# Optimization experiments

Hardware: AMD Instinct MI355X
Metric: run time of the kernel (lower is better)

## Reference

```python
import jax, jax.numpy as jnp
import numpy as np

N_QUBITS = 10


def _apply_1q(state, U, wire, n):
    # state: (B, 2**n) complex; apply 2x2 U on `wire` (wire 0 = most significant bit)
    B = state.shape[0]
    left = 2 ** wire
    right = 2 ** (n - wire - 1)
    s = state.reshape(B, left, 2, right)
    s = jnp.einsum('ij,bljr->blir', U, s)
    return s.reshape(B, 2 ** n)


def _cnot(state, c, t, n):
    # CNOT with control wire c, target wire t
    B = state.shape[0]
    s = state.reshape((B,) + (2,) * n)
    ci, ti = c + 1, t + 1
    flipped = jnp.flip(s, axis=ti)
    zero = jnp.take(s, 0, axis=ci)      # control=0 slice unchanged
    one = jnp.take(flipped, 1, axis=ci)  # control=1 slice with target flipped
    s = jnp.stack([zero, one], axis=ci)
    return s.reshape(B, 2 ** n)


def _rot_matrix(phi, theta, omega):
    # PennyLane Rot(phi, theta, omega) = RZ(omega) @ RY(theta) @ RZ(phi)
    c = jnp.cos(theta / 2).astype(jnp.complex64)
    s = jnp.sin(theta / 2).astype(jnp.complex64)
    ep = jnp.exp(-0.5j * (phi + omega).astype(jnp.complex64))  # e^{-i(phi+omega)/2}
    em = jnp.exp(0.5j * (phi - omega).astype(jnp.complex64))   # e^{ i(phi-omega)/2}
    row0 = jnp.stack([ep * c, -em * s])
    row1 = jnp.stack([jnp.conj(em) * s, jnp.conj(ep) * c])
    return jnp.stack([row0, row1])  # (2, 2)


def setup_inputs() -> dict:
    key = jax.random.key(0)
    k1, k2 = jax.random.split(key)
    B, dim = 8192, 2 ** N_QUBITS
    patch = jax.random.normal(k1, (B, dim), dtype=jnp.float32)
    patch = patch / jnp.linalg.norm(patch, axis=1, keepdims=True)  # L2-normalized amplitudes
    weights = 0.01 * jax.random.normal(k2, (N_QUBITS, 3), dtype=jnp.float32)
    return {"patch_batch": patch, "weights": weights}


def reference(patch_batch, weights):
    n = weights.shape[0]
    state = patch_batch.astype(jnp.complex64)  # amplitude embedding
    for w in range(n):
        U = _rot_matrix(weights[w, 0], weights[w, 1], weights[w, 2])
        state = _apply_1q(state, U, w, n)
    for w in range(n - 1):
        state = _cnot(state, w, w + 1, n)
    state = _cnot(state, n - 1, 0, n)
    # expectation values of X, Y, Z on wire 0
    s2 = state.reshape(-1, 2, 2 ** (n - 1))
    a0, a1 = s2[:, 0], s2[:, 1]
    z = jnp.sum(jnp.conj(a0) * a1, axis=1)
    ex = 2.0 * jnp.real(z)
    ey = 2.0 * jnp.imag(z)
    ez = jnp.sum(jnp.abs(a0) ** 2 - jnp.abs(a1) ** 2, axis=1)
    out = jnp.stack([ex, ey, ez], axis=1)  # (B, 3)
    return jnp.nan_to_num(out, nan=0.0, posinf=1.0, neginf=-1.0)
```

## Files before the change

### kernel.cpp

```cpp
#include <hip/hip_runtime.h>


__global__ void qk_setup_gates(const float* __restrict__ w, float* __restrict__ U) {
    int i = threadIdx.x;
    if (i < 10) {
        float phi = w[3 * i + 0];
        float th  = w[3 * i + 1];
        float om  = w[3 * i + 2];
        float c  = cosf(0.5f * th), s  = sinf(0.5f * th);
        float hp = 0.5f * (phi + om), hm = 0.5f * (phi - om);
        float chp = cosf(hp), shp = sinf(hp);
        float chm = cosf(hm), shm = sinf(hm);
        float* u = U + 8 * i;
        u[0] =  c * chp;  u[1] = -c * shp;
        u[2] = -s * chm;  u[3] = -s * shm;
        u[4] =  s * chm;  u[5] = -s * shm;
        u[6] =  c * chp;  u[7] =  c * shp;
    }
}

__global__ __launch_bounds__(256) void qk_sim(const float* __restrict__ x,
                                              const float* __restrict__ Ug,
                                              float* __restrict__ out,
                                              int nstates) {
    int wave = (int)((blockIdx.x * blockDim.x + threadIdx.x) >> 6);
    int lane = threadIdx.x & 63;
    if (wave >= nstates) return;

    const float4* row = (const float4*)(x + (size_t)wave * 1024);
    float re[16], im[16];
#pragma unroll
    for (int k = 0; k < 4; k++) {
        float4 v = row[lane * 4 + k];
        re[4 * k + 0] = v.x; re[4 * k + 1] = v.y;
        re[4 * k + 2] = v.z; re[4 * k + 3] = v.w;
        im[4 * k + 0] = 0.f; im[4 * k + 1] = 0.f;
        im[4 * k + 2] = 0.f; im[4 * k + 3] = 0.f;
    }

#pragma unroll
    for (int rb = 0; rb < 4; rb++) {
        const float* u = Ug + 8 * (9 - rb);
        float u0 = u[0], u1 = u[1], u2 = u[2], u3 = u[3];
        float u4 = u[4], u5 = u[5], u6 = u[6], u7 = u[7];
#pragma unroll
        for (int r0 = 0; r0 < 16; r0++) {
            if (r0 & (1 << rb)) continue;
            int r1 = r0 | (1 << rb);
            float ar = re[r0], ai = im[r0];
            float br = re[r1], bi = im[r1];
            re[r0] = u0 * ar - u1 * ai + u2 * br - u3 * bi;
            im[r0] = u0 * ai + u1 * ar + u2 * bi + u3 * br;
            re[r1] = u4 * ar - u5 * ai + u6 * br - u7 * bi;
            im[r1] = u4 * ai + u5 * ar + u6 * bi + u7 * br;
        }
    }

#pragma unroll
    for (int l = 0; l < 6; l++) {
        const float* u = Ug + 8 * (5 - l);
        int bit = (lane >> l) & 1;
        float Ar = bit ? u[6] : u[0];
        float Ai = bit ? u[7] : u[1];
        float Br = bit ? u[4] : u[2];
        float Bi = bit ? u[5] : u[3];
#pragma unroll
        for (int r = 0; r < 16; r++) {
            float mr = re[r], mi = im[r];
            float pr = __shfl_xor(mr, 1 << l, 64);
            float pi = __shfl_xor(mi, 1 << l, 64);
            re[r] = Ar * mr - Ai * mi + Br * pr - Bi * pi;
            im[r] = Ar * mi + Ai * mr + Br * pi + Bi * pr;
        }
    }

    float ex = 0.f, ey = 0.f, ez = 0.f;
    int lpar = __popc(lane & 31) & 1;
#pragma unroll
    for (int r = 0; r < 16; r++) {
        float mr = re[r], mi = im[r];
        float pr = __shfl_xor(mr, 48, 64);
        float pi = __shfl_xor(mi, 48, 64);
        float sgn = ((lpar ^ (__popc(r) & 1)) != 0) ? -1.f : 1.f;
        ex += mr * pr + mi * pi;
        ey += sgn * (mr * pi - mi * pr);
        ez += sgn * (mr * mr + mi * mi);
    }
#pragma unroll
    for (int off = 32; off >= 1; off >>= 1) {
        ex += __shfl_xor(ex, off, 64);
        ey += __shfl_xor(ey, off, 64);
        ez += __shfl_xor(ez, off, 64);
    }
    if (lane == 0) {
        float* o = out + 3 * (size_t)wave;
        o[0] = ex; o[1] = ey; o[2] = ez;
    }
}

extern "C" void kernel_launch(void* const* d_in, const int* in_sizes, int n_in,
                              void* d_out, int out_size, void* d_ws, size_t ws_size,
                              hipStream_t stream) {
    const float* patch   = (const float*)d_in[0];
    const float* weights = (const float*)d_in[1];
    float* out = (float*)d_out;
    float* Ug  = (float*)d_ws;

    int nstates = in_sizes[0] / 1024;

    qk_setup_gates<<<1, 64, 0, stream>>>(weights, Ug);

    int waves_per_block = 256 / 64;
    int nblocks = (nstates + waves_per_block - 1) / waves_per_block;
    qk_sim<<<nblocks, 256, 0, stream>>>(patch, Ug, out, nstates);
}
```

Before: 94.98 us.

## Factor Rot gates into diagonal phases plus real RY rotations

Each Rot gate is split into its RZ phase parts and a real RY rotation. The RZ(phi) phases act on a real input state, so they fold into one precomputed per-lane and per-register phase multiply at load time. The RY butterflies become real 2x2 mixes, roughly quartering the FLOPs per amplitude pair, and the final RZ(omega) phases are applied only to the partial sums of the wire-0 expectations. The block count also drops its rounding-up, so the launch assumes the state count is a multiple of four.

Result: no change. 93.89 us (-1.1%).

```diff
diff --git a/kernel.cpp b/kernel.cpp
--- a/kernel.cpp
+++ b/kernel.cpp
@@ -1,100 +1,120 @@
 #include <hip/hip_runtime.h>
 
 
-__global__ void qk_setup_gates(const float* __restrict__ w, float* __restrict__ U) {
-    int i = threadIdx.x;
-    if (i < 10) {
-        float phi = w[3 * i + 0];
-        float th  = w[3 * i + 1];
-        float om  = w[3 * i + 2];
-        float c  = cosf(0.5f * th), s  = sinf(0.5f * th);
-        float hp = 0.5f * (phi + om), hm = 0.5f * (phi - om);
-        float chp = cosf(hp), shp = sinf(hp);
-        float chm = cosf(hm), shm = sinf(hm);
-        float* u = U + 8 * i;
-        u[0] =  c * chp;  u[1] = -c * shp;
-        u[2] = -s * chm;  u[3] = -s * shm;
-        u[4] =  s * chm;  u[5] = -s * shm;
-        u[6] =  c * chp;  u[7] =  c * shp;
+__global__ void qk_setup(const float* __restrict__ w, float* __restrict__ ws) {
+    int t = threadIdx.x;
+    if (t < 10) {
+        float th = w[3 * t + 1];
+        ws[2 * t]     = cosf(0.5f * th);
+        ws[2 * t + 1] = sinf(0.5f * th);
+    }
+    if (t < 16) {
+        float a = 0.f;
+        for (int j = 0; j < 4; j++) if ((t >> j) & 1) a += w[3 * (9 - j)];
+        ws[32 + 2 * t]     = cosf(a);
+        ws[32 + 2 * t + 1] = sinf(a);
+    }
+    {
+        float a = 0.f;
+        for (int j = 0; j < 6; j++) if ((t >> j) & 1) a += w[3 * (5 - j)];
+        ws[64 + 2 * t]     = cosf(a);
+        ws[64 + 2 * t + 1] = sinf(a);
+    }
+    if (t < 4) {
+        float d = (1.f - 2.f * ((t >> 1) & 1)) * w[2] + (1.f - 2.f * (t & 1)) * w[5];
+        ws[192 + 2 * t]     = cosf(d);
+        ws[192 + 2 * t + 1] = sinf(d);
     }
 }
 
 __global__ __launch_bounds__(256) void qk_sim(const float* __restrict__ x,
-                                              const float* __restrict__ Ug,
+                                              const float* __restrict__ ws,
                                               float* __restrict__ out,
                                               int nstates) {
     int wave = (int)((blockIdx.x * blockDim.x + threadIdx.x) >> 6);
     int lane = threadIdx.x & 63;
     if (wave >= nstates) return;
 
+    const float* CS = ws;
+    const float* R  = ws + 32;
+    const float* L  = ws + 64;
+    const float* T4 = ws + 192;
+
+    float Lr = L[2 * lane], Li = L[2 * lane + 1];
+
     const float4* row = (const float4*)(x + (size_t)wave * 1024);
     float re[16], im[16];
 #pragma unroll
     for (int k = 0; k < 4; k++) {
         float4 v = row[lane * 4 + k];
-        re[4 * k + 0] = v.x; re[4 * k + 1] = v.y;
-        re[4 * k + 2] = v.z; re[4 * k + 3] = v.w;
-        im[4 * k + 0] = 0.f; im[4 * k + 1] = 0.f;
-        im[4 * k + 2] = 0.f; im[4 * k + 3] = 0.f;
+        float xs0 = v.x, xs1 = v.y, xs2 = v.z, xs3 = v.w;
+        float xv[4] = {xs0, xs1, xs2, xs3};
+#pragma unroll
+        for (int j = 0; j < 4; j++) {
+            int r = 4 * k + j;
+            float ar = xv[j] * R[2 * r];
+            float ai = xv[j] * R[2 * r + 1];
+            re[r] = Lr * ar - Li * ai;
+            im[r] = Lr * ai + Li * ar;
+        }
     }
 
 #pragma unroll
     for (int rb = 0; rb < 4; rb++) {
-        const float* u = Ug + 8 * (9 - rb);
-        float u0 = u[0], u1 = u[1], u2 = u[2], u3 = u[3];
-        float u4 = u[4], u5 = u[5], u6 = u[6], u7 = u[7];
+        float c = CS[2 * (9 - rb)], s = CS[2 * (9 - rb) + 1];
 #pragma unroll
         for (int r0 = 0; r0 < 16; r0++) {
             if (r0 & (1 << rb)) continue;
             int r1 = r0 | (1 << rb);
-            float ar = re[r0], ai = im[r0];
-            float br = re[r1], bi = im[r1];
-            re[r0] = u0 * ar - u1 * ai + u2 * br - u3 * bi;
-            im[r0] = u0 * ai + u1 * ar + u2 * bi + u3 * br;
-            re[r1] = u4 * ar - u5 * ai + u6 * br - u7 * bi;
-            im[r1] = u4 * ai + u5 * ar + u6 * bi + u7 * br;
+            float a0r = re[r0], a0i = im[r0];
+            float a1r = re[r1], a1i = im[r1];
+            re[r0] = c * a0r - s * a1r;  im[r0] = c * a0i - s * a1i;
+            re[r1] = s * a0r + c * a1r;  im[r1] = s * a0i + c * a1i;
         }
     }
 
 #pragma unroll
     for (int l = 0; l < 6; l++) {
-        const float* u = Ug + 8 * (5 - l);
-        int bit = (lane >> l) & 1;
-        float Ar = bit ? u[6] : u[0];
-        float Ai = bit ? u[7] : u[1];
-        float Br = bit ? u[4] : u[2];
-        float Bi = bit ? u[5] : u[3];
+        float c = CS[2 * (5 - l)], s = CS[2 * (5 - l) + 1];
+        float ss = ((lane >> l) & 1) ? s : -s;
 #pragma unroll
         for (int r = 0; r < 16; r++) {
             float mr = re[r], mi = im[r];
             float pr = __shfl_xor(mr, 1 << l, 64);
             float pi = __shfl_xor(mi, 1 << l, 64);
-            re[r] = Ar * mr - Ai * mi + Br * pr - Bi * pi;
-            im[r] = Ar * mi + Ai * mr + Br * pi + Bi * pr;
+            re[r] = c * mr + ss * pr;
+            im[r] = c * mi + ss * pi;
         }
     }
 
-    float ex = 0.f, ey = 0.f, ez = 0.f;
-    int lpar = __popc(lane & 31) & 1;
+    float zxr = 0.f, zxi = 0.f, zyr = 0.f, zyi = 0.f, ez = 0.f;
 #pragma unroll
     for (int r = 0; r < 16; r++) {
         float mr = re[r], mi = im[r];
         float pr = __shfl_xor(mr, 48, 64);
         float pi = __shfl_xor(mi, 48, 64);
-        float sgn = ((lpar ^ (__popc(r) & 1)) != 0) ? -1.f : 1.f;
-        ex += mr * pr + mi * pi;
-        ey += sgn * (mr * pi - mi * pr);
-        ez += sgn * (mr * mr + mi * mi);
+        float cr = mr * pr + mi * pi;
+        float ci = mr * pi - mi * pr;
+        zxr += cr; zxi += ci;
+        if (__popc(r) & 1) { zyr -= cr; zyi -= ci; ez -= mr * mr + mi * mi; }
+        else               { zyr += cr; zyi += ci; ez += mr * mr + mi * mi; }
     }
+    int j4 = (lane >> 4) & 3;
+    float cD = T4[2 * j4], sD = T4[2 * j4 + 1];
+    float lsgn = (__popc(lane & 31) & 1) ? -1.f : 1.f;
+    float ex  = cD * zxr - sD * zxi;
+    float ey  = lsgn * (cD * zyi + sD * zyr);
+    float ezl = lsgn * ez;
+
 #pragma unroll
     for (int off = 32; off >= 1; off >>= 1) {
-        ex += __shfl_xor(ex, off, 64);
-        ey += __shfl_xor(ey, off, 64);
-        ez += __shfl_xor(ez, off, 64);
+        ex  += __shfl_xor(ex,  off, 64);
+        ey  += __shfl_xor(ey,  off, 64);
+        ezl += __shfl_xor(ezl, off, 64);
     }
     if (lane == 0) {
         float* o = out + 3 * (size_t)wave;
-        o[0] = ex; o[1] = ey; o[2] = ez;
+        o[0] = ex; o[1] = ey; o[2] = ezl;
     }
 }
 
@@ -104,13 +124,12 @@
     const float* patch   = (const float*)d_in[0];
     const float* weights = (const float*)d_in[1];
     float* out = (float*)d_out;
-    float* Ug  = (float*)d_ws;
+    float* ws  = (float*)d_ws;
 
     int nstates = in_sizes[0] / 1024;
 
-    qk_setup_gates<<<1, 64, 0, stream>>>(weights, Ug);
+    qk_setup<<<1, 64, 0, stream>>>(weights, ws);
 
-    int waves_per_block = 256 / 64;
-    int nblocks = (nstates + waves_per_block - 1) / waves_per_block;
-    qk_sim<<<nblocks, 256, 0, stream>>>(patch, Ug, out, nstates);
+    int nblocks = nstates / 4;
+    qk_sim<<<nblocks, 256, 0, stream>>>(patch, ws, out, nstates);
 }
```
